# Performance work log

Measured on AMD Instinct MI355X. Metric: run time of the kernel, lower is better.

## Reference

```python
import jax, jax.numpy as jnp
import numpy as np

N = 400_000
B = 64          # number of segments (point clouds)
IN_C = 128
INTER = (256, 512, 512)
OUT_C = 512


def setup_inputs() -> dict:
    key = jax.random.key(0)
    ks = jax.random.split(key, 12)
    pos_emd = jax.random.normal(ks[0], (N, IN_C), dtype=jnp.float32)
    radius_p_batch = jnp.sort(jax.random.randint(ks[1], (N,), 0, B))

    def lin(k, fin, fout):
        kw, kb = jax.random.split(k)
        s = 1.0 / np.sqrt(fin)
        W = jax.random.uniform(kw, (fin, fout), jnp.float32, -s, s)
        b = jax.random.uniform(kb, (fout,), jnp.float32, -s, s)
        return W, b

    W1, b1 = lin(ks[2], IN_C, INTER[0])
    W2, b2 = lin(ks[3], INTER[0], INTER[1])
    W3, b3 = lin(ks[4], INTER[1], INTER[2])
    W4, b4 = lin(ks[5], IN_C + INTER[2], OUT_C)
    W5, b5 = lin(ks[6], OUT_C, OUT_C)
    return {
        "pos_emd": pos_emd, "radius_p_batch": radius_p_batch,
        "W1": W1, "b1": b1, "W2": W2, "b2": b2, "W3": W3, "b3": b3,
        "W4": W4, "b4": b4, "W5": W5, "b5": b5,
    }


def reference(pos_emd, radius_p_batch, W1, b1, W2, b2, W3, b3, W4, b4, W5, b5):
    # mlp1: Linear-ReLU-Linear-ReLU-Linear
    h = jax.nn.relu(pos_emd @ W1 + b1)
    h = jax.nn.relu(h @ W2 + b2)
    h = h @ W3 + b3                              # [N, 512]
    # global max pool over segments
    g = jax.ops.segment_max(h, radius_p_batch, num_segments=B)  # [B, 512]
    # broadcast each segment's global feature back to its points (ids sorted)
    g_rep = g[radius_p_batch]                    # [N, 512]
    z = jnp.concatenate((pos_emd, g_rep), axis=-1)  # [N, 640]
    # mlp2: Linear-ReLU-Linear
    z = jax.nn.relu(z @ W4 + b4)
    z = z @ W5 + b5                              # [N, 512]
    return jax.ops.segment_max(z, radius_p_batch, num_segments=B)  # [B, 512]
```

## Files before the change

### kernel.cpp

```cpp
#include <hip/hip_runtime.h>
#include <stdint.h>


typedef __bf16 bf16;
typedef __bf16 bf16x4 __attribute__((ext_vector_type(4)));
typedef __bf16 bf16x8 __attribute__((ext_vector_type(8)));
typedef float f32x4 __attribute__((ext_vector_type(4)));
typedef __attribute__((address_space(3))) char lds_char;

#define N_PTS 400000
#define ORD_NEG_INF 0x007FFFFFu

__device__ __forceinline__ unsigned f2ord(float f) {
  unsigned u = __float_as_uint(f);
  return (u & 0x80000000u) ? ~u : (u | 0x80000000u);
}
__device__ __forceinline__ float ord2f(unsigned o) {
  unsigned u = (o & 0x80000000u) ? (o ^ 0x80000000u) : ~o;
  return __uint_as_float(u);
}

__device__ __forceinline__ void gld16(const bf16* g, lds_char* l) {
  __builtin_amdgcn_global_load_lds((const __attribute__((address_space(1))) void*)g,
                                   (__attribute__((address_space(3))) void*)l, 16, 0, 0);
}

#define DSR(dst, preg, IMM) \
  asm volatile("ds_read_b128 %0, %1 offset:%c2" : "=&v"(dst) : "v"(preg), "n"(IMM))

#define SCHED0 __builtin_amdgcn_sched_barrier(0)
#define LGKM0 do { asm volatile("s_waitcnt lgkmcnt(0)"); SCHED0; } while (0)
#define LGKM4 do { asm volatile("s_waitcnt lgkmcnt(4)"); SCHED0; } while (0)
#define SBARR do { __builtin_amdgcn_s_barrier(); SCHED0; } while (0)
#define VMW0 do { asm volatile("s_waitcnt vmcnt(0)"); SCHED0; } while (0)

__global__ void k_init(unsigned* g_ord, unsigned* out_u) {
  int i = blockIdx.x * 256 + threadIdx.x;
  if (i < 64 * 512) { g_ord[i] = ORD_NEG_INF; out_u[i] = ORD_NEG_INF; }
}

__global__ void k_convX(const float* __restrict__ x, bf16* __restrict__ y, long n4) {
  long i = (long)blockIdx.x * 256 + threadIdx.x;
  long stride = (long)gridDim.x * 256;
  for (; i < n4; i += stride) {
    float4 v = ((const float4*)x)[i];
    bf16x4 o = {(bf16)v.x, (bf16)v.y, (bf16)v.z, (bf16)v.w};
    ((bf16x4*)y)[i] = o;
  }
}

__global__ void k_convWt(const float* __restrict__ W, bf16* __restrict__ Wt, int K, int Nout) {
  int idx = blockIdx.x * 256 + threadIdx.x;
  if (idx < K * Nout) {
    int k = idx / Nout, c = idx - k * Nout;
    Wt[(size_t)c * K + k] = (bf16)W[idx];
  }
}

__global__ void k_segbias(const unsigned* __restrict__ g_ord, const float* __restrict__ W4,
                          const float* __restrict__ b4, float* __restrict__ sb) {
  const int s = blockIdx.x, c = threadIdx.x;
  __shared__ float gs[512];
  gs[c] = ord2f(g_ord[s * 512 + c]);
  __syncthreads();
  float acc = b4[c];
  for (int j = 0; j < 512; ++j) acc = fmaf(gs[j], W4[(size_t)(128 + j) * 512 + c], acc);
  sb[s * 512 + c] = acc;
}

__global__ void k_decode(unsigned* p, int n) {
  int i = blockIdx.x * 256 + threadIdx.x;
  if (i < n) { float f = ord2f(p[i]); ((float*)p)[i] = f; }
}

template <int BIASMODE, bool RELU, int EPI, int K, int NOUT>
__launch_bounds__(256, 2)
__global__ void k_gemm(const bf16* __restrict__ A, const bf16* __restrict__ Bt,
                       const float* __restrict__ bias, const int* __restrict__ ids,
                       long row_off, bf16* __restrict__ out,
                       unsigned* __restrict__ outAtomic) {
  constexpr int NT = K / 32;
  constexpr int NBX = NOUT / 128;
  __shared__ __align__(16) char sMem[49152];
  __shared__ int sIds[256];
  const int tid = threadIdx.x;
  const int wid = tid >> 6, lane = tid & 63;
  const int wr = wid >> 1, wc = wid & 1;
  const int lr = lane & 15, lk = lane >> 4;

  const int orig = (int)blockIdx.y * NBX + (int)blockIdx.x;
  const int gidm = orig / NBX, gn = orig - gidm * NBX;
  const int nwgm = (int)gridDim.y;
  const int q = nwgm >> 3, r = nwgm & 7;
  const int xcd = gidm & 7, lid = gidm >> 3;
  const int wgm = (xcd < r ? xcd * (q + 1) : r * (q + 1) + (xcd - r) * q) + lid;
  const int m0 = wgm * 256;
  const int n0 = gn * 128;

  if constexpr (BIASMODE == 1 || EPI == 1) {
    long gi = row_off + m0 + tid;
    if (gi > (long)N_PTS - 1) gi = (long)N_PTS - 1;
    sIds[tid] = ids[gi];
  }
  SCHED0;

  lds_char* lds3 = (lds_char*)sMem;

  const int rIn = lane >> 2;
  const int cblk = ((lane & 3) ^ ((lane >> 3) & 3)) * 8;
  const bf16* srcA[4]; lds_char* dstA[4];
  const bf16* srcB[2]; lds_char* dstB[2];
#pragma unroll
  for (int k = 0; k < 4; ++k) {
    const int g8 = wid * 4 + k;
    srcA[k] = A + (size_t)(m0 + g8 * 16 + rIn) * K + cblk;
    dstA[k] = lds3 + g8 * 1024 + lane * 16;
  }
#pragma unroll
  for (int k = 0; k < 2; ++k) {
    const int g8 = wid * 2 + k;
    srcB[k] = Bt + (size_t)(n0 + g8 * 16 + rIn) * K + cblk;
    dstB[k] = lds3 + 16384 + g8 * 1024 + lane * 16;
  }
  auto STG = [&](int tau) {
    if (tau < NT) {
      const int bo = (tau & 1) * 24576;
      const int ko = tau * 32;
#pragma unroll
      for (int k = 0; k < 4; ++k) gld16(srcA[k] + ko, dstA[k] + bo);
#pragma unroll
      for (int k = 0; k < 2; ++k) gld16(srcB[k] + ko, dstB[k] + bo);
    }
  };

  const unsigned sl16 = (((unsigned)lk) ^ ((unsigned)(lr >> 1) & 3u)) * 16u;
  lds_char* vA = lds3 + wr * 8192 + lr * 64 + sl16;
  lds_char* vB = lds3 + 16384 + wc * 4096 + lr * 64 + sl16;

  bf16x8 aR[8], bR[4];
  f32x4 acc[8][4];
#pragma unroll
  for (int i = 0; i < 8; ++i)
#pragma unroll
    for (int j = 0; j < 4; ++j) acc[i][j] = {0.f, 0.f, 0.f, 0.f};

#define MM8(ILO) do { __builtin_amdgcn_s_setprio(1); \
  _Pragma("unroll") for (int i_ = 0; i_ < 4; ++i_) \
  _Pragma("unroll") for (int j_ = 0; j_ < 4; ++j_) \
    acc[(ILO) + i_][j_] = __builtin_amdgcn_mfma_f32_16x16x32_bf16(aR[(ILO) + i_], bR[j_], acc[(ILO) + i_][j_], 0, 0, 0); \
  __builtin_amdgcn_s_setprio(0); } while (0)

  STG(0);
  asm volatile("s_waitcnt vmcnt(0) lgkmcnt(0)");
  SCHED0;
  SBARR;

#pragma unroll 1
  for (int t = 0; t < NT; ++t) {
    STG(t + 1);
    lds_char* pA = vA + (t & 1) * 24576;
    lds_char* pB = vB + (t & 1) * 24576;
    DSR(bR[0], pB, 0); DSR(bR[1], pB, 1024); DSR(bR[2], pB, 2048); DSR(bR[3], pB, 3072);
    DSR(aR[0], pA, 0); DSR(aR[1], pA, 1024); DSR(aR[2], pA, 2048); DSR(aR[3], pA, 3072);
    DSR(aR[4], pA, 4096); DSR(aR[5], pA, 5120); DSR(aR[6], pA, 6144); DSR(aR[7], pA, 7168);
    LGKM4;
    MM8(0);
    LGKM0;
    MM8(4);
    if (t < NT - 1) {
      VMW0;
      SBARR;
    }
  }
#undef MM8

  if constexpr (EPI == 0) {
#pragma unroll
    for (int j = 0; j < 4; ++j) {
      const int col = n0 + wc * 64 + j * 16 + lr;
      float bcol = (BIASMODE == 0) ? bias[col] : 0.f;
#pragma unroll
      for (int i = 0; i < 8; ++i) {
#pragma unroll
        for (int q2 = 0; q2 < 4; ++q2) {
          const int rl = wr * 128 + i * 16 + lk * 4 + q2;
          float v = acc[i][j][q2];
          if constexpr (BIASMODE == 0) v += bcol;
          else v += bias[(size_t)sIds[rl] * 512 + col];
          if constexpr (RELU) v = fmaxf(v, 0.f);
          out[(size_t)(m0 + rl) * NOUT + col] = (bf16)v;
        }
      }
    }
  } else {
    const int sLo = sIds[wr * 128], sHi = sIds[wr * 128 + 127];
#pragma unroll
    for (int j = 0; j < 4; ++j) {
      const int col = n0 + wc * 64 + j * 16 + lr;
      const float bcol = bias[col];
      for (int s = sLo; s <= sHi; ++s) {
        float m = -__builtin_inff();
#pragma unroll
        for (int i = 0; i < 8; ++i)
#pragma unroll
          for (int q2 = 0; q2 < 4; ++q2) {
            const int rl = wr * 128 + i * 16 + lk * 4 + q2;
            const bool rv = (row_off + m0 + rl) < (long)N_PTS;
            float v = acc[i][j][q2] + bcol;
            m = (sIds[rl] == s && rv) ? fmaxf(m, v) : m;
          }
        m = fmaxf(m, __shfl_xor(m, 16));
        m = fmaxf(m, __shfl_xor(m, 32));
        if (lane < 16) atomicMax(&outAtomic[(size_t)s * 512 + col], f2ord(m));
      }
    }
  }
}

static inline long lmin(long a, long b) { return a < b ? a : b; }

extern "C" void kernel_launch(void* const* d_in, const int* in_sizes, int n_in,
                              void* d_out, int out_size, void* d_ws, size_t ws_size,
                              hipStream_t stream) {
  const float* pos = (const float*)d_in[0];
  const int* ids = (const int*)d_in[1];
  const float* W1 = (const float*)d_in[2]; const float* b1 = (const float*)d_in[3];
  const float* W2 = (const float*)d_in[4]; const float* b2 = (const float*)d_in[5];
  const float* W3 = (const float*)d_in[6]; const float* b3 = (const float*)d_in[7];
  const float* W4 = (const float*)d_in[8]; const float* b4 = (const float*)d_in[9];
  const float* W5 = (const float*)d_in[10]; const float* b5 = (const float*)d_in[11];

  char* ws = (char*)d_ws;
  size_t off = 0;
  auto alloc = [&](size_t bytes) -> char* {
    off = (off + 255) & ~(size_t)255;
    char* p = ws + off; off += bytes; return p;
  };
  bf16* Wt1  = (bf16*)alloc(128 * 256 * 2);
  bf16* Wt2  = (bf16*)alloc(256 * 512 * 2);
  bf16* Wt3  = (bf16*)alloc(512 * 512 * 2);
  bf16* Wt4a = (bf16*)alloc(128 * 512 * 2);
  bf16* Wt5  = (bf16*)alloc(512 * 512 * 2);
  unsigned* g_ord = (unsigned*)alloc(64 * 512 * 4);
  float* sb = (float*)alloc(64 * 512 * 4);
  bf16* Xbf = (bf16*)alloc((size_t)(N_PTS + 384) * 128 * 2);

  const size_t per_row = (256 + 512) * 2;
  size_t fixed_end = (off + 255) & ~(size_t)255;
  long avail = (long)ws_size - (long)fixed_end - 8192;
  long maxrows = avail / (long)per_row;
  long chunk = (maxrows - 256) & ~255L;
  if (chunk > N_PTS) chunk = N_PTS;
  if (chunk < 256) chunk = 256;
  long rows_alloc = chunk + 256;

  bf16* h1 = (bf16*)alloc((size_t)rows_alloc * 256 * 2);
  bf16* h2 = (bf16*)alloc((size_t)rows_alloc * 512 * 2);

  k_init<<<dim3(128), dim3(256), 0, stream>>>(g_ord, (unsigned*)d_out);
  k_convWt<<<dim3((128 * 256 + 255) / 256), dim3(256), 0, stream>>>(W1, Wt1, 128, 256);
  k_convWt<<<dim3((256 * 512 + 255) / 256), dim3(256), 0, stream>>>(W2, Wt2, 256, 512);
  k_convWt<<<dim3((512 * 512 + 255) / 256), dim3(256), 0, stream>>>(W3, Wt3, 512, 512);
  k_convWt<<<dim3((128 * 512 + 255) / 256), dim3(256), 0, stream>>>(W4, Wt4a, 128, 512);
  k_convWt<<<dim3((512 * 512 + 255) / 256), dim3(256), 0, stream>>>(W5, Wt5, 512, 512);
  k_convX<<<dim3(2048), dim3(256), 0, stream>>>(pos, Xbf, (long)N_PTS * 32);

  for (long o = 0; o < N_PTS; o += chunk) {
    long rows = lmin(chunk, N_PTS - o);
    unsigned mb = (unsigned)((rows + 255) / 256);
    k_gemm<0, true, 0, 128, 256><<<dim3(2, mb), dim3(256), 0, stream>>>(Xbf + o * 128, Wt1, b1, ids, o, h1, nullptr);
    k_gemm<0, true, 0, 256, 512><<<dim3(4, mb), dim3(256), 0, stream>>>(h1, Wt2, b2, ids, o, h2, nullptr);
    k_gemm<0, false, 1, 512, 512><<<dim3(4, mb), dim3(256), 0, stream>>>(h2, Wt3, b3, ids, o, nullptr, g_ord);
  }
  k_segbias<<<dim3(64), dim3(512), 0, stream>>>(g_ord, W4, b4, sb);
  for (long o = 0; o < N_PTS; o += chunk) {
    long rows = lmin(chunk, N_PTS - o);
    unsigned mb = (unsigned)((rows + 255) / 256);
    k_gemm<1, true, 0, 128, 512><<<dim3(4, mb), dim3(256), 0, stream>>>(Xbf + o * 128, Wt4a, sb, ids, o, h2, nullptr);
    k_gemm<0, false, 1, 512, 512><<<dim3(4, mb), dim3(256), 0, stream>>>(h2, Wt5, b5, ids, o, nullptr, (unsigned*)d_out);
  }
  k_decode<<<dim3(128), dim3(256), 0, stream>>>((unsigned*)d_out, 64 * 512);
}
```

Measured before the change: 1.198 ms.

## Shrink GEMM tile to 128x128 with 3 blocks per CU and flat XCD remap

Cuts the GEMM workgroup tile from 256x128 to 128x128, which halves the accumulator registers and LDS staging (32 KB instead of 48 KB) so launch bounds can target three workgroups per CU. The XCD-aware block remap now runs over the flattened grid, and LDS fragment reads are issued before the next stage's global-to-LDS prefetch, with a single wait before all MFMAs. The aim is higher occupancy and better latency hiding. The cost is less operand reuse per tile, so more global and LDS traffic per FLOP, and more atomic epilogue work because there are twice as many row tiles.

```diff
diff --git a/kernel.cpp b/kernel.cpp
--- a/kernel.cpp
+++ b/kernel.cpp
@@ -30,7 +30,6 @@
 
 #define SCHED0 __builtin_amdgcn_sched_barrier(0)
 #define LGKM0 do { asm volatile("s_waitcnt lgkmcnt(0)"); SCHED0; } while (0)
-#define LGKM4 do { asm volatile("s_waitcnt lgkmcnt(4)"); SCHED0; } while (0)
 #define SBARR do { __builtin_amdgcn_s_barrier(); SCHED0; } while (0)
 #define VMW0 do { asm volatile("s_waitcnt vmcnt(0)"); SCHED0; } while (0)
 
@@ -74,33 +73,34 @@
 }
 
 template <int BIASMODE, bool RELU, int EPI, int K, int NOUT>
-__launch_bounds__(256, 2)
+__launch_bounds__(256, 3)
 __global__ void k_gemm(const bf16* __restrict__ A, const bf16* __restrict__ Bt,
                        const float* __restrict__ bias, const int* __restrict__ ids,
                        long row_off, bf16* __restrict__ out,
                        unsigned* __restrict__ outAtomic) {
   constexpr int NT = K / 32;
   constexpr int NBX = NOUT / 128;
-  __shared__ __align__(16) char sMem[49152];
-  __shared__ int sIds[256];
+  __shared__ __align__(16) char sMem[32768];
+  __shared__ int sIds[128];
   const int tid = threadIdx.x;
   const int wid = tid >> 6, lane = tid & 63;
   const int wr = wid >> 1, wc = wid & 1;
   const int lr = lane & 15, lk = lane >> 4;
 
+  const int nwg = NBX * (int)gridDim.y;
   const int orig = (int)blockIdx.y * NBX + (int)blockIdx.x;
-  const int gidm = orig / NBX, gn = orig - gidm * NBX;
-  const int nwgm = (int)gridDim.y;
-  const int q = nwgm >> 3, r = nwgm & 7;
-  const int xcd = gidm & 7, lid = gidm >> 3;
-  const int wgm = (xcd < r ? xcd * (q + 1) : r * (q + 1) + (xcd - r) * q) + lid;
-  const int m0 = wgm * 256;
-  const int n0 = gn * 128;
+  const int q = nwg >> 3, r = nwg & 7;
+  const int xcd = orig & 7, lid = orig >> 3;
+  const int wg = (xcd < r ? xcd * (q + 1) : r * (q + 1) + (xcd - r) * q) + lid;
+  const int n0 = (wg % NBX) * 128;
+  const int m0 = (wg / NBX) * 128;
 
   if constexpr (BIASMODE == 1 || EPI == 1) {
-    long gi = row_off + m0 + tid;
-    if (gi > (long)N_PTS - 1) gi = (long)N_PTS - 1;
-    sIds[tid] = ids[gi];
+    if (tid < 128) {
+      long gi = row_off + m0 + tid;
+      if (gi > (long)N_PTS - 1) gi = (long)N_PTS - 1;
+      sIds[tid] = ids[gi];
+    }
   }
   SCHED0;
 
@@ -108,47 +108,37 @@
 
   const int rIn = lane >> 2;
   const int cblk = ((lane & 3) ^ ((lane >> 3) & 3)) * 8;
-  const bf16* srcA[4]; lds_char* dstA[4];
+  const bf16* srcA[2]; lds_char* dstA[2];
   const bf16* srcB[2]; lds_char* dstB[2];
 #pragma unroll
-  for (int k = 0; k < 4; ++k) {
-    const int g8 = wid * 4 + k;
+  for (int k = 0; k < 2; ++k) {
+    const int g8 = wid * 2 + k;
     srcA[k] = A + (size_t)(m0 + g8 * 16 + rIn) * K + cblk;
     dstA[k] = lds3 + g8 * 1024 + lane * 16;
-  }
-#pragma unroll
-  for (int k = 0; k < 2; ++k) {
-    const int g8 = wid * 2 + k;
     srcB[k] = Bt + (size_t)(n0 + g8 * 16 + rIn) * K + cblk;
-    dstB[k] = lds3 + 16384 + g8 * 1024 + lane * 16;
+    dstB[k] = lds3 + 8192 + g8 * 1024 + lane * 16;
   }
   auto STG = [&](int tau) {
     if (tau < NT) {
-      const int bo = (tau & 1) * 24576;
+      const int bo = (tau & 1) * 16384;
       const int ko = tau * 32;
 #pragma unroll
-      for (int k = 0; k < 4; ++k) gld16(srcA[k] + ko, dstA[k] + bo);
+      for (int k = 0; k < 2; ++k) gld16(srcA[k] + ko, dstA[k] + bo);
 #pragma unroll
       for (int k = 0; k < 2; ++k) gld16(srcB[k] + ko, dstB[k] + bo);
     }
   };
 
   const unsigned sl16 = (((unsigned)lk) ^ ((unsigned)(lr >> 1) & 3u)) * 16u;
-  lds_char* vA = lds3 + wr * 8192 + lr * 64 + sl16;
-  lds_char* vB = lds3 + 16384 + wc * 4096 + lr * 64 + sl16;
-
-  bf16x8 aR[8], bR[4];
-  f32x4 acc[8][4];
-#pragma unroll
-  for (int i = 0; i < 8; ++i)
+  lds_char* vA = lds3 + wr * 4096 + lr * 64 + sl16;
+  lds_char* vB = lds3 + 8192 + wc * 4096 + lr * 64 + sl16;
+
+  bf16x8 aR[4], bR[4];
+  f32x4 acc[4][4];
+#pragma unroll
+  for (int i = 0; i < 4; ++i)
 #pragma unroll
     for (int j = 0; j < 4; ++j) acc[i][j] = {0.f, 0.f, 0.f, 0.f};
-
-#define MM8(ILO) do { __builtin_amdgcn_s_setprio(1); \
-  _Pragma("unroll") for (int i_ = 0; i_ < 4; ++i_) \
-  _Pragma("unroll") for (int j_ = 0; j_ < 4; ++j_) \
-    acc[(ILO) + i_][j_] = __builtin_amdgcn_mfma_f32_16x16x32_bf16(aR[(ILO) + i_], bR[j_], acc[(ILO) + i_][j_], 0, 0, 0); \
-  __builtin_amdgcn_s_setprio(0); } while (0)
 
   STG(0);
   asm volatile("s_waitcnt vmcnt(0) lgkmcnt(0)");
@@ -157,22 +147,24 @@
 
 #pragma unroll 1
   for (int t = 0; t < NT; ++t) {
+    lds_char* pA = vA + (t & 1) * 16384;
+    lds_char* pB = vB + (t & 1) * 16384;
+    DSR(aR[0], pA, 0); DSR(aR[1], pA, 1024); DSR(aR[2], pA, 2048); DSR(aR[3], pA, 3072);
+    DSR(bR[0], pB, 0); DSR(bR[1], pB, 1024); DSR(bR[2], pB, 2048); DSR(bR[3], pB, 3072);
     STG(t + 1);
-    lds_char* pA = vA + (t & 1) * 24576;
-    lds_char* pB = vB + (t & 1) * 24576;
-    DSR(bR[0], pB, 0); DSR(bR[1], pB, 1024); DSR(bR[2], pB, 2048); DSR(bR[3], pB, 3072);
-    DSR(aR[0], pA, 0); DSR(aR[1], pA, 1024); DSR(aR[2], pA, 2048); DSR(aR[3], pA, 3072);
-    DSR(aR[4], pA, 4096); DSR(aR[5], pA, 5120); DSR(aR[6], pA, 6144); DSR(aR[7], pA, 7168);
-    LGKM4;
-    MM8(0);
     LGKM0;
-    MM8(4);
+    __builtin_amdgcn_s_setprio(1);
+#pragma unroll
+    for (int i = 0; i < 4; ++i)
+#pragma unroll
+      for (int j = 0; j < 4; ++j)
+        acc[i][j] = __builtin_amdgcn_mfma_f32_16x16x32_bf16(aR[i], bR[j], acc[i][j], 0, 0, 0);
+    __builtin_amdgcn_s_setprio(0);
     if (t < NT - 1) {
       VMW0;
       SBARR;
     }
   }
-#undef MM8
 
   if constexpr (EPI == 0) {
 #pragma unroll
@@ -180,10 +172,10 @@
       const int col = n0 + wc * 64 + j * 16 + lr;
       float bcol = (BIASMODE == 0) ? bias[col] : 0.f;
 #pragma unroll
-      for (int i = 0; i < 8; ++i) {
+      for (int i = 0; i < 4; ++i) {
 #pragma unroll
         for (int q2 = 0; q2 < 4; ++q2) {
-          const int rl = wr * 128 + i * 16 + lk * 4 + q2;
+          const int rl = wr * 64 + i * 16 + lk * 4 + q2;
           float v = acc[i][j][q2];
           if constexpr (BIASMODE == 0) v += bcol;
           else v += bias[(size_t)sIds[rl] * 512 + col];
@@ -193,7 +185,7 @@
       }
     }
   } else {
-    const int sLo = sIds[wr * 128], sHi = sIds[wr * 128 + 127];
+    const int sLo = sIds[wr * 64], sHi = sIds[wr * 64 + 63];
 #pragma unroll
     for (int j = 0; j < 4; ++j) {
       const int col = n0 + wc * 64 + j * 16 + lr;
@@ -201,10 +193,10 @@
       for (int s = sLo; s <= sHi; ++s) {
         float m = -__builtin_inff();
 #pragma unroll
-        for (int i = 0; i < 8; ++i)
+        for (int i = 0; i < 4; ++i)
 #pragma unroll
           for (int q2 = 0; q2 < 4; ++q2) {
-            const int rl = wr * 128 + i * 16 + lk * 4 + q2;
+            const int rl = wr * 64 + i * 16 + lk * 4 + q2;
             const bool rv = (row_off + m0 + rl) < (long)N_PTS;
             float v = acc[i][j][q2] + bcol;
             m = (sIds[rl] == s && rv) ? fmaxf(m, v) : m;
@@ -267,7 +259,7 @@
 
   for (long o = 0; o < N_PTS; o += chunk) {
     long rows = lmin(chunk, N_PTS - o);
-    unsigned mb = (unsigned)((rows + 255) / 256);
+    unsigned mb = (unsigned)((rows + 127) / 128);
     k_gemm<0, true, 0, 128, 256><<<dim3(2, mb), dim3(256), 0, stream>>>(Xbf + o * 128, Wt1, b1, ids, o, h1, nullptr);
     k_gemm<0, true, 0, 256, 512><<<dim3(4, mb), dim3(256), 0, stream>>>(h1, Wt2, b2, ids, o, h2, nullptr);
     k_gemm<0, false, 1, 512, 512><<<dim3(4, mb), dim3(256), 0, stream>>>(h2, Wt3, b3, ids, o, nullptr, g_ord);
@@ -275,7 +267,7 @@
   k_segbias<<<dim3(64), dim3(512), 0, stream>>>(g_ord, W4, b4, sb);
   for (long o = 0; o < N_PTS; o += chunk) {
     long rows = lmin(chunk, N_PTS - o);
-    unsigned mb = (unsigned)((rows + 255) / 256);
+    unsigned mb = (unsigned)((rows + 127) / 128);
     k_gemm<1, true, 0, 128, 512><<<dim3(4, mb), dim3(256), 0, stream>>>(Xbf + o * 128, Wt4a, sb, ids, o, h2, nullptr);
     k_gemm<0, false, 1, 512, 512><<<dim3(4, mb), dim3(256), 0, stream>>>(h2, Wt5, b5, ids, o, nullptr, (unsigned*)d_out);
   }
```

New measurement: 1.200 ms. Within noise of the previous version (+0.2%).
